# Kernel optimization log

Measured on AMD Instinct MI355X. Metric: run time of the kernel, lower is better.

The kernel has to match this reference:

```python
import jax, jax.numpy as jnp
import numpy as np

N_SEND = 100000   # sender nodes
N_RECV = 100000   # receiver nodes
E = 600000        # edges
D = 128           # node feature channels (128x0e)
A = 8             # attr channels (8x0e)
S = 64            # edge scalar dim = fc_neurons[0]
H = 128           # fc hidden = fc_neurons[1]; tp.weight_numel = 128
NUM_NEIGHBORS = 32.0
SILU_NORM = 1.679177  # e3nn normalize2mom constant for silu: (E[silu(N(0,1))^2])^-0.5


def fctp(x, y, W):
    """e3nn FullyConnectedTensorProduct for all-scalar (0e) irreps:
    single 'uvw' path, path weight 1/sqrt(mul_u*mul_v)."""
    return jnp.einsum('nu,nv,uvw->nw', x, y, W) / np.sqrt(x.shape[1] * y.shape[1]).astype(np.float32)


def setup_inputs() -> dict:
    key = jax.random.key(0)
    ks = jax.random.split(key, 14)
    return {
        'sender_input': jax.random.normal(ks[0], (N_SEND, D), jnp.float32),
        'sender_attr': jax.random.normal(ks[1], (N_SEND, A), jnp.float32),
        'receiver_input': jax.random.normal(ks[2], (N_RECV, D), jnp.float32),
        'receiver_attr': jax.random.normal(ks[3], (N_RECV, A), jnp.float32),
        'edge_src': jax.random.randint(ks[4], (E,), 0, N_SEND, jnp.int32),
        'edge_dst': jax.random.randint(ks[5], (E,), 0, N_RECV, jnp.int32),
        'edge_attr': jax.random.normal(ks[6], (E, 1), jnp.float32),
        'edge_scalars': jax.random.normal(ks[7], (E, S), jnp.float32),
        # e3nn TP weights are initialized N(0,1)
        'W_sc': jax.random.normal(ks[8], (D, A, D), jnp.float32),
        'W_lin1': jax.random.normal(ks[9], (D, A, D), jnp.float32),
        'W_fc1': jax.random.normal(ks[10], (S, H), jnp.float32),
        'W_fc2': jax.random.normal(ks[11], (H, D), jnp.float32),
        'W_lin2': jax.random.normal(ks[12], (D, A, D), jnp.float32),
        'W_lin3': jax.random.normal(ks[13], (D, A, 1), jnp.float32),
    }


def reference(sender_input, sender_attr, receiver_input, receiver_attr,
              edge_src, edge_dst, edge_attr, edge_scalars,
              W_sc, W_lin1, W_fc1, W_fc2, W_lin2, W_lin3):
    # FullyConnectedNet([S, H, weight_numel], silu): act(x@W/sqrt(fan_in)), last layer linear
    h = SILU_NORM * jax.nn.silu(edge_scalars @ W_fc1 / np.sqrt(S).astype(np.float32))
    weight = h @ W_fc2 / np.sqrt(H).astype(np.float32)                     # [E, D] per-edge TP weights

    receiver_self_connection = fctp(receiver_input, receiver_attr, W_sc)   # [Nr, D]
    sender_features = fctp(sender_input, sender_attr, W_lin1)              # [Ns, D]

    # gather -> per-edge weighted ('uvu') tensor product with 1x0e edge_attr -> scatter-add
    edge_features = weight * sender_features[edge_src] * edge_attr         # [E, D]
    receiver_features = jax.ops.segment_sum(edge_features, edge_dst,
                                            num_segments=receiver_input.shape[0])
    receiver_features = receiver_features / np.sqrt(NUM_NEIGHBORS).astype(np.float32)

    receiver_conv_out = fctp(receiver_features, receiver_attr, W_lin2)     # [Nr, D]
    receiver_angle = 0.1 * fctp(receiver_features, receiver_attr, W_lin3)  # [Nr, 1]
    # sc.output_mask is all-ones for this irreps config, so sin gating applies to all channels
    return jnp.cos(receiver_angle) * receiver_self_connection + jnp.sin(receiver_angle) * receiver_conv_out
```

## Files before the change

### kernel.cpp

```cpp
#include <hip/hip_runtime.h>
#include <hip/hip_bf16.h>
#include <math.h>

#define NS 100000
#define NR 100000
#define NE 600000
#define SILU_NORM 1.679177f

typedef __attribute__((ext_vector_type(8))) short short8;
typedef __attribute__((ext_vector_type(4))) float f32x4;

static __device__ __forceinline__ short f2bf(float f) {
    return __builtin_bit_cast(short, __float2bfloat16(f));
}

#define GLDS16(g, l)                                                         \
    __builtin_amdgcn_global_load_lds(                                        \
        (const __attribute__((address_space(1))) unsigned int*)(const void*)(g), \
        (__attribute__((address_space(3))) unsigned int*)(void*)(l), 16, 0, 0)

__global__ void swz_kernel(const float* __restrict__ W,
                           __hip_bfloat16* __restrict__ out, int total)
{
    int idx = blockIdx.x * 256 + threadIdx.x;
    if (idx >= total) return;
    int s = idx >> 12, r = idx & 4095;
    int f = r >> 9;  r &= 511;
    int quad = r >> 7; r &= 127;
    int wl = r >> 3;
    int j = r & 7;
    int k = s * 32 + quad * 8 + j;
    int w = f * 16 + wl;
    out[idx] = __float2bfloat16(W[(size_t)k * 128 + w]);
}

__global__ __launch_bounds__(256) void hist_kernel(const int* __restrict__ edst,
                                                   int* __restrict__ cnt)
{
    int i = blockIdx.x * 256 + threadIdx.x;
    if (i < NE) atomicAdd(&cnt[edst[i]], 1);
}

#define SCAN_BLK 1024

__global__ __launch_bounds__(256) void scan1_kernel(const int* __restrict__ cnt,
                                                    int* __restrict__ bsum, int n)
{
    __shared__ int ts[256];
    int b = blockIdx.x, t = threadIdx.x;
    int base = b * SCAN_BLK + t * 4;
    int s = 0;
    #pragma unroll
    for (int k = 0; k < 4; ++k) { int i = base + k; if (i < n) s += cnt[i]; }
    ts[t] = s; __syncthreads();
    #pragma unroll
    for (int off = 128; off; off >>= 1) {
        if (t < off) ts[t] += ts[t + off];
        __syncthreads();
    }
    if (t == 0) bsum[b] = ts[0];
}

__global__ __launch_bounds__(128) void scan2_kernel(const int* __restrict__ bsum,
                                                    int* __restrict__ bofs, int nb)
{
    __shared__ int sh[128];
    int t = threadIdx.x;
    sh[t] = (t < nb) ? bsum[t] : 0;
    __syncthreads();
    for (int off = 1; off < 128; off <<= 1) {
        int v = (t >= off) ? sh[t - off] : 0;
        __syncthreads();
        sh[t] += v;
        __syncthreads();
    }
    if (t < nb) bofs[t] = (t == 0) ? 0 : sh[t - 1];
}

__global__ __launch_bounds__(256) void scan3_kernel(const int* __restrict__ cnt,
                                                    const int* __restrict__ bofs,
                                                    int* __restrict__ ofs, int n)
{
    __shared__ int ts[256];
    int b = blockIdx.x, t = threadIdx.x;
    int base = b * SCAN_BLK + t * 4;
    int v[4]; int s = 0;
    #pragma unroll
    for (int k = 0; k < 4; ++k) {
        int i = base + k;
        v[k] = (i < n) ? cnt[i] : 0;
        s += v[k];
    }
    ts[t] = s; __syncthreads();
    for (int off = 1; off < 256; off <<= 1) {
        int u = (t >= off) ? ts[t - off] : 0;
        __syncthreads();
        ts[t] += u;
        __syncthreads();
    }
    int run = bofs[b] + ts[t] - s;
    #pragma unroll
    for (int k = 0; k < 4; ++k) {
        int i = base + k;
        if (i < n) ofs[i] = run;
        run += v[k];
    }
}

__global__ __launch_bounds__(256) void scatter_kernel(const int* __restrict__ edst,
                                                      int* __restrict__ ofs,
                                                      int* __restrict__ perm)
{
    int i = blockIdx.x * 256 + threadIdx.x;
    if (i < NE) {
        int pos = atomicAdd(&ofs[edst[i]], 1);
        perm[pos] = i;
    }
}

__global__ __launch_bounds__(256) void fctp_mfma_kernel(
    const float* __restrict__ x, const float* __restrict__ y,
    const __hip_bfloat16* __restrict__ Wswz, float* __restrict__ out,
    float scale, int N)
{
    __shared__ __hip_bfloat16 Wb[2][8192];
    __shared__ float xs[2][128 * 8];

    const int tid = threadIdx.x;
    const int lane = tid & 63;
    const int wv = tid >> 6;
    const int quad = lane >> 4;
    const int wl = lane & 15;
    const int n0 = blockIdx.x * 128;

    float ya[2][8];
    #pragma unroll
    for (int mt = 0; mt < 2; ++mt) {
        int node = n0 + wv * 32 + mt * 16 + wl;
        if (node >= N) node = N - 1;
        const float4* yp = (const float4*)(y + (size_t)node * 8);
        float4 a = yp[0], b = yp[1];
        ya[mt][0] = a.x; ya[mt][1] = a.y; ya[mt][2] = a.z; ya[mt][3] = a.w;
        ya[mt][4] = b.x; ya[mt][5] = b.y; ya[mt][6] = b.z; ya[mt][7] = b.w;
    }

    f32x4 acc[2][8];
    #pragma unroll
    for (int mt = 0; mt < 2; ++mt)
        #pragma unroll
        for (int f = 0; f < 8; ++f)
            acc[mt][f] = (f32x4){0.f, 0.f, 0.f, 0.f};

    auto stage = [&](int b, int cc) {
        const char* src = (const char*)(Wswz + (size_t)cc * 8192);
        #pragma unroll
        for (int i = 0; i < 4; ++i) {
            int off = (i * 256 + tid) * 16;
            GLDS16(src + off, (char*)Wb[b] + off);
        }
        int nl = tid >> 1, c4 = (tid & 1) * 4;
        int node = n0 + nl;
        if (node >= N) node = N - 1;
        GLDS16(x + (size_t)node * 128 + cc * 8 + c4, (char*)xs[b] + tid * 16);
    };

    stage(0, 0);
    __syncthreads();

    for (int cc = 0; cc < 16; ++cc) {
        int cur = cc & 1;
        if (cc < 15) stage(cur ^ 1, cc + 1);

        #pragma unroll
        for (int ks = 0; ks < 2; ++ks) {
            short8 bfr[8];
            #pragma unroll
            for (int f = 0; f < 8; ++f)
                bfr[f] = *(const short8*)((const short*)Wb[cur] +
                                          (size_t)ks * 4096 + (f * 64 + lane) * 8);
            #pragma unroll
            for (int mt = 0; mt < 2; ++mt) {
                float xv = xs[cur][(wv * 32 + mt * 16 + wl) * 8 + ks * 4 + quad];
                short8 af;
                #pragma unroll
                for (int v = 0; v < 8; ++v) af[v] = f2bf(xv * ya[mt][v]);
                #pragma unroll
                for (int f = 0; f < 8; ++f)
                    acc[mt][f] = __builtin_amdgcn_mfma_f32_16x16x32_bf16(
                        af, bfr[f], acc[mt][f], 0, 0, 0);
            }
        }
        __syncthreads();
    }

    #pragma unroll
    for (int mt = 0; mt < 2; ++mt) {
        #pragma unroll
        for (int r = 0; r < 4; ++r) {
            int node = n0 + wv * 32 + mt * 16 + quad * 4 + r;
            if (node < N) {
                #pragma unroll
                for (int f = 0; f < 8; ++f)
                    out[(size_t)node * 128 + f * 16 + wl] = acc[mt][f][r] * scale;
            }
        }
    }
}

__global__ __launch_bounds__(256, 4) void edge_mfma_kernel(
    const int* __restrict__ esrc, const int* __restrict__ edst,
    const float* __restrict__ eattr, const float* __restrict__ escal,
    const int* __restrict__ perm,
    const __hip_bfloat16* __restrict__ W1swz,
    const __hip_bfloat16* __restrict__ W2swz,
    const float* __restrict__ sf, float* __restrict__ rfeat)
{
    __shared__ __hip_bfloat16 hA[16384];

    const int tid = threadIdx.x;
    const int lane = tid & 63;
    const int wv = tid >> 6;
    const int quad = lane >> 4;
    const int wl = lane & 15;
    const int e0 = blockIdx.x * 128;

    int epm[2];
    #pragma unroll
    for (int mt = 0; mt < 2; ++mt) {
        int j = e0 + (wv * 2 + mt) * 16 + wl;
        if (j >= NE) j = NE - 1;
        epm[mt] = perm[j];
    }

    short8 af1[2][2];
    #pragma unroll
    for (int ks = 0; ks < 2; ++ks)
        #pragma unroll
        for (int mt = 0; mt < 2; ++mt) {
            const float4* p = (const float4*)(escal + (size_t)epm[mt] * 64 +
                                              ks * 32 + quad * 8);
            float4 a = p[0], b = p[1];
            short8 v;
            v[0] = f2bf(a.x); v[1] = f2bf(a.y); v[2] = f2bf(a.z); v[3] = f2bf(a.w);
            v[4] = f2bf(b.x); v[5] = f2bf(b.y); v[6] = f2bf(b.z); v[7] = f2bf(b.w);
            af1[ks][mt] = v;
        }

    f32x4 acc1[2][8];
    #pragma unroll
    for (int mt = 0; mt < 2; ++mt)
        #pragma unroll
        for (int f = 0; f < 8; ++f) acc1[mt][f] = (f32x4){0.f, 0.f, 0.f, 0.f};

    #pragma unroll
    for (int ks = 0; ks < 2; ++ks)
        #pragma unroll
        for (int f = 0; f < 8; ++f) {
            short8 bfr = *(const short8*)((const short*)W1swz +
                                          (size_t)ks * 4096 + (f * 64 + lane) * 8);
            acc1[0][f] = __builtin_amdgcn_mfma_f32_16x16x32_bf16(
                af1[0][0], bfr, acc1[0][f], 0, 0, 0);
            acc1[1][f] = __builtin_amdgcn_mfma_f32_16x16x32_bf16(
                af1[0][1], bfr, acc1[1][f], 0, 0, 0);
        }

    #pragma unroll
    for (int mt = 0; mt < 2; ++mt)
        #pragma unroll
        for (int f = 0; f < 8; ++f) acc1[mt][f] = (f32x4){0.f, 0.f, 0.f, 0.f};
    #pragma unroll
    for (int ks = 0; ks < 2; ++ks)
        #pragma unroll
        for (int f = 0; f < 8; ++f) {
            short8 bfr = *(const short8*)((const short*)W1swz +
                                          (size_t)ks * 4096 + (f * 64 + lane) * 8);
            acc1[0][f] = __builtin_amdgcn_mfma_f32_16x16x32_bf16(
                af1[ks][0], bfr, acc1[0][f], 0, 0, 0);
            acc1[1][f] = __builtin_amdgcn_mfma_f32_16x16x32_bf16(
                af1[ks][1], bfr, acc1[1][f], 0, 0, 0);
        }

    #pragma unroll
    for (int mt = 0; mt < 2; ++mt) {
        int MT = wv * 2 + mt;
        #pragma unroll
        for (int f = 0; f < 8; ++f) {
            int s2 = f >> 1;
            int q2 = ((f & 1) * 2 + (wl >> 3)) & 3;
            int j2 = wl & 7;
            #pragma unroll
            for (int r = 0; r < 4; ++r) {
                float t = acc1[mt][f][r] * 0.125f;
                float h = SILU_NORM * t / (1.f + __expf(-t));
                int lpos = q2 * 16 + quad * 4 + r;
                ((short*)hA)[((size_t)(s2 * 8 + MT) * 64 + lpos) * 8 + j2] = f2bf(h);
            }
        }
    }
    __syncthreads();

    f32x4 acc2[2][8];
    #pragma unroll
    for (int mt = 0; mt < 2; ++mt)
        #pragma unroll
        for (int f = 0; f < 8; ++f) acc2[mt][f] = (f32x4){0.f, 0.f, 0.f, 0.f};

    #pragma unroll
    for (int ks = 0; ks < 4; ++ks) {
        short8 afA = *(const short8*)((const short*)hA +
                                      ((size_t)(ks * 8 + wv * 2 + 0) * 64 + lane) * 8);
        short8 afB = *(const short8*)((const short*)hA +
                                      ((size_t)(ks * 8 + wv * 2 + 1) * 64 + lane) * 8);
        #pragma unroll
        for (int f = 0; f < 8; ++f) {
            short8 bfr = *(const short8*)((const short*)W2swz +
                                          (size_t)ks * 4096 + (f * 64 + lane) * 8);
            acc2[0][f] = __builtin_amdgcn_mfma_f32_16x16x32_bf16(
                afA, bfr, acc2[0][f], 0, 0, 0);
            acc2[1][f] = __builtin_amdgcn_mfma_f32_16x16x32_bf16(
                afB, bfr, acc2[1][f], 0, 0, 0);
        }
    }

    const float s128 = 0.08838834764831845f;
    #pragma unroll
    for (int mt = 0; mt < 2; ++mt) {
        int jbase = e0 + (wv * 2 + mt) * 16 + quad * 4;
        if (jbase < NE) {
            int4 pj = *(const int4*)(perm + jbase);
            int dsts[4], srcs[4];
            float eas[4];
            #pragma unroll
            for (int r = 0; r < 4; ++r) {
                int e = (r == 0) ? pj.x : (r == 1) ? pj.y : (r == 2) ? pj.z : pj.w;
                dsts[r] = edst[e];
                srcs[r] = esrc[e];
                eas[r]  = eattr[e] * s128;
            }
            float run[8];
            int curdst = dsts[0];
            #pragma unroll
            for (int f = 0; f < 8; ++f)
                run[f] = acc2[mt][f][0] * eas[0] *
                         sf[(size_t)srcs[0] * 128 + f * 16 + wl];
            #pragma unroll
            for (int r = 1; r < 4; ++r) {
                float val[8];
                #pragma unroll
                for (int f = 0; f < 8; ++f)
                    val[f] = acc2[mt][f][r] * eas[r] *
                             sf[(size_t)srcs[r] * 128 + f * 16 + wl];
                if (dsts[r] == curdst) {
                    #pragma unroll
                    for (int f = 0; f < 8; ++f) run[f] += val[f];
                } else {
                    #pragma unroll
                    for (int f = 0; f < 8; ++f)
                        atomicAdd(&rfeat[(size_t)curdst * 128 + f * 16 + wl], run[f]);
                    curdst = dsts[r];
                    #pragma unroll
                    for (int f = 0; f < 8; ++f) run[f] = val[f];
                }
            }
            #pragma unroll
            for (int f = 0; f < 8; ++f)
                atomicAdd(&rfeat[(size_t)curdst * 128 + f * 16 + wl], run[f]);
        }
    }
}

__global__ __launch_bounds__(256) void conv_fuse_kernel(
    const float* __restrict__ x, const float* __restrict__ y,
    const __hip_bfloat16* __restrict__ Wswz, const float* __restrict__ W3,
    const float* __restrict__ rsc, float* __restrict__ out, int N)
{
    __shared__ __hip_bfloat16 Wb[2][8192];
    __shared__ float xs[2][128 * 8];

    const int tid = threadIdx.x;
    const int lane = tid & 63;
    const int wv = tid >> 6;
    const int quad = lane >> 4;
    const int wl = lane & 15;
    const int n0 = blockIdx.x * 128;

    float ya[2][8];
    #pragma unroll
    for (int mt = 0; mt < 2; ++mt) {
        int node = n0 + wv * 32 + mt * 16 + wl;
        if (node >= N) node = N - 1;
        const float4* yp = (const float4*)(y + (size_t)node * 8);
        float4 a = yp[0], b = yp[1];
        ya[mt][0] = a.x; ya[mt][1] = a.y; ya[mt][2] = a.z; ya[mt][3] = a.w;
        ya[mt][4] = b.x; ya[mt][5] = b.y; ya[mt][6] = b.z; ya[mt][7] = b.w;
    }

    f32x4 acc[2][8];
    #pragma unroll
    for (int mt = 0; mt < 2; ++mt)
        #pragma unroll
        for (int f = 0; f < 8; ++f)
            acc[mt][f] = (f32x4){0.f, 0.f, 0.f, 0.f};
    float aacc[2] = {0.f, 0.f};

    auto stage = [&](int b, int cc) {
        const char* src = (const char*)(Wswz + (size_t)cc * 8192);
        #pragma unroll
        for (int i = 0; i < 4; ++i) {
            int off = (i * 256 + tid) * 16;
            GLDS16(src + off, (char*)Wb[b] + off);
        }
        int nl = tid >> 1, c4 = (tid & 1) * 4;
        int node = n0 + nl;
        if (node >= N) node = N - 1;
        GLDS16(x + (size_t)node * 128 + cc * 8 + c4, (char*)xs[b] + tid * 16);
    };

    stage(0, 0);
    __syncthreads();

    for (int cc = 0; cc < 16; ++cc) {
        int cur = cc & 1;
        if (cc < 15) stage(cur ^ 1, cc + 1);

        #pragma unroll
        for (int ks = 0; ks < 2; ++ks) {
            short8 bfr[8];
            #pragma unroll
            for (int f = 0; f < 8; ++f)
                bfr[f] = *(const short8*)((const short*)Wb[cur] +
                                          (size_t)ks * 4096 + (f * 64 + lane) * 8);
            const float4* wp = (const float4*)(W3 + ((cc * 8 + ks * 4 + quad) * 8));
            float4 w3a = wp[0], w3b = wp[1];
            float w3v[8] = {w3a.x, w3a.y, w3a.z, w3a.w, w3b.x, w3b.y, w3b.z, w3b.w};
            #pragma unroll
            for (int mt = 0; mt < 2; ++mt) {
                float xv = xs[cur][(wv * 32 + mt * 16 + wl) * 8 + ks * 4 + quad];
                short8 af;
                #pragma unroll
                for (int v = 0; v < 8; ++v) {
                    float pr = xv * ya[mt][v];
                    af[v] = f2bf(pr);
                    aacc[mt] += pr * w3v[v];
                }
                #pragma unroll
                for (int f = 0; f < 8; ++f)
                    acc[mt][f] = __builtin_amdgcn_mfma_f32_16x16x32_bf16(
                        af, bfr[f], acc[mt][f], 0, 0, 0);
            }
        }
        __syncthreads();
    }

    float ared[2];
    #pragma unroll
    for (int mt = 0; mt < 2; ++mt) {
        float a = aacc[mt];
        a += __shfl_xor(a, 16);
        a += __shfl_xor(a, 32);
        ared[mt] = a * 5.524271728019903e-4f;
    }

    const float cs = 5.524271728019903e-3f;
    #pragma unroll
    for (int mt = 0; mt < 2; ++mt) {
        #pragma unroll
        for (int r = 0; r < 4; ++r) {
            int node = n0 + wv * 32 + mt * 16 + quad * 4 + r;
            float a = __shfl(ared[mt], quad * 4 + r);
            if (node < N) {
                float ca = __cosf(a), sa = __sinf(a);
                #pragma unroll
                for (int f = 0; f < 8; ++f) {
                    size_t o = (size_t)node * 128 + f * 16 + wl;
                    out[o] = ca * rsc[o] + sa * (acc[mt][f][r] * cs);
                }
            }
        }
    }
}

extern "C" void kernel_launch(void* const* d_in, const int* in_sizes, int n_in,
                              void* d_out, int out_size, void* d_ws, size_t ws_size,
                              hipStream_t stream)
{
    const float* sender_input   = (const float*)d_in[0];
    const float* sender_attr    = (const float*)d_in[1];
    const float* receiver_input = (const float*)d_in[2];
    const float* receiver_attr  = (const float*)d_in[3];
    const int*   edge_src  = (const int*)d_in[4];
    const int*   edge_dst  = (const int*)d_in[5];
    const float* edge_attr = (const float*)d_in[6];
    const float* edge_scal = (const float*)d_in[7];
    const float* W_sc   = (const float*)d_in[8];
    const float* W_lin1 = (const float*)d_in[9];
    const float* W_fc1  = (const float*)d_in[10];
    const float* W_fc2  = (const float*)d_in[11];
    const float* W_lin2 = (const float*)d_in[12];
    const float* W_lin3 = (const float*)d_in[13];

    char* ws = (char*)d_ws;
    float* sf    = (float*)(ws);
    float* rfeat = (float*)(ws + 51200000);
    __hip_bfloat16* Wl1s = (__hip_bfloat16*)(ws + 102400000);
    __hip_bfloat16* Wscs = (__hip_bfloat16*)(ws + 102662144);
    __hip_bfloat16* Wl2s = (__hip_bfloat16*)(ws + 102924288);
    __hip_bfloat16* W1s  = (__hip_bfloat16*)(ws + 103186432);
    __hip_bfloat16* W2s  = (__hip_bfloat16*)(ws + 103202816);
    float* rsc = sf;

    int* perm = (int*)d_out;
    int* cnt  = (int*)d_out + 600000;
    int* ofs  = (int*)d_out + 700000;
    int* bsum = (int*)d_out + 800000;
    int* bofs = (int*)d_out + 800128;

    swz_kernel<<<512, 256, 0, stream>>>(W_lin1, Wl1s, 131072);
    swz_kernel<<<512, 256, 0, stream>>>(W_sc,   Wscs, 131072);
    swz_kernel<<<512, 256, 0, stream>>>(W_lin2, Wl2s, 131072);
    swz_kernel<<<32,  256, 0, stream>>>(W_fc1,  W1s,  8192);
    swz_kernel<<<64,  256, 0, stream>>>(W_fc2,  W2s,  16384);

    hipMemsetAsync(rfeat, 0, (size_t)NR * 128 * 4, stream);
    hipMemsetAsync(cnt, 0, (size_t)NR * 4, stream);

    const int nbScan = (NR + SCAN_BLK - 1) / SCAN_BLK;
    hist_kernel<<<(NE + 255) / 256, 256, 0, stream>>>(edge_dst, cnt);
    scan1_kernel<<<nbScan, 256, 0, stream>>>(cnt, bsum, NR);
    scan2_kernel<<<1, 128, 0, stream>>>(bsum, bofs, nbScan);
    scan3_kernel<<<nbScan, 256, 0, stream>>>(cnt, bofs, ofs, NR);
    scatter_kernel<<<(NE + 255) / 256, 256, 0, stream>>>(edge_dst, ofs, perm);

    fctp_mfma_kernel<<<(NS + 127) / 128, 256, 0, stream>>>(
        sender_input, sender_attr, Wl1s, sf, 0.03125f, NS);
    edge_mfma_kernel<<<(NE + 127) / 128, 256, 0, stream>>>(
        edge_src, edge_dst, edge_attr, edge_scal, perm, W1s, W2s, sf, rfeat);
    fctp_mfma_kernel<<<(NR + 127) / 128, 256, 0, stream>>>(
        receiver_input, receiver_attr, Wscs, rsc, 0.03125f, NR);
    conv_fuse_kernel<<<(NR + 127) / 128, 256, 0, stream>>>(
        rfeat, receiver_attr, Wl2s, W_lin3, rsc, (float*)d_out, NR);
}
```

Baseline: 698.3 us.

## Keep edge MLP hidden in registers via transposed MFMA, pre-sort edge metadata

Computes the first FC layer transposed (weights as A operand) so the SiLU output lands directly in the register layout needed as the A fragment of the second MFMA, with W_fc2 re-swizzled to match. This removes the shared-memory staging buffer and the block barrier. The scatter kernel now also writes dst, src and edge_attr in sorted order, so the edge kernel reads them with contiguous vector loads instead of gathering through perm. The duplicated first-layer MFMA pass is removed, sender-feature gathers are issued up front, and launch bounds drop to 3 blocks per SM to give more registers.

```diff
diff --git a/kernel.cpp b/kernel.cpp
--- a/kernel.cpp
+++ b/kernel.cpp
@@ -34,6 +34,21 @@
     out[idx] = __float2bfloat16(W[(size_t)k * 128 + w]);
 }
 
+__global__ void swz2pi_kernel(const float* __restrict__ W,
+                              __hip_bfloat16* __restrict__ out, int total)
+{
+    int idx = blockIdx.x * 256 + threadIdx.x;
+    if (idx >= total) return;
+    int s = idx >> 12, r = idx & 4095;
+    int f = r >> 9;  r &= 511;
+    int quad = r >> 7; r &= 127;
+    int wl = r >> 3;
+    int j = r & 7;
+    int c = 32 * s + 16 * (j >> 2) + 4 * quad + (j & 3);
+    int w = f * 16 + wl;
+    out[idx] = __float2bfloat16(W[(size_t)c * 128 + w]);
+}
+
 __global__ __launch_bounds__(256) void hist_kernel(const int* __restrict__ edst,
                                                    int* __restrict__ cnt)
 {
@@ -107,14 +122,20 @@
     }
 }
 
-__global__ __launch_bounds__(256) void scatter_kernel(const int* __restrict__ edst,
-                                                      int* __restrict__ ofs,
-                                                      int* __restrict__ perm)
+__global__ __launch_bounds__(256) void scatter_kernel(
+    const int* __restrict__ edst, const int* __restrict__ esrc,
+    const float* __restrict__ eattr, int* __restrict__ ofs,
+    int* __restrict__ perm, int* __restrict__ edst_s,
+    int* __restrict__ esrc_s, float* __restrict__ eattr_s)
 {
     int i = blockIdx.x * 256 + threadIdx.x;
     if (i < NE) {
-        int pos = atomicAdd(&ofs[edst[i]], 1);
+        int d = edst[i];
+        int pos = atomicAdd(&ofs[d], 1);
         perm[pos] = i;
+        edst_s[pos] = d;
+        esrc_s[pos] = esrc[i];
+        eattr_s[pos] = eattr[i];
     }
 }
 
@@ -207,16 +228,14 @@
     }
 }
 
-__global__ __launch_bounds__(256, 4) void edge_mfma_kernel(
-    const int* __restrict__ esrc, const int* __restrict__ edst,
-    const float* __restrict__ eattr, const float* __restrict__ escal,
-    const int* __restrict__ perm,
+__global__ __launch_bounds__(256, 3) void edge_mfma_kernel(
+    const int* __restrict__ perm, const int* __restrict__ edst_s,
+    const int* __restrict__ esrc_s, const float* __restrict__ eattr_s,
+    const float* __restrict__ escal,
     const __hip_bfloat16* __restrict__ W1swz,
     const __hip_bfloat16* __restrict__ W2swz,
     const float* __restrict__ sf, float* __restrict__ rfeat)
 {
-    __shared__ __hip_bfloat16 hA[16384];
-
     const int tid = threadIdx.x;
     const int lane = tid & 63;
     const int wv = tid >> 6;
@@ -230,6 +249,20 @@
         int j = e0 + (wv * 2 + mt) * 16 + wl;
         if (j >= NE) j = NE - 1;
         epm[mt] = perm[j];
+    }
+
+    const float s128 = 0.08838834764831845f;
+    int4 dstv[2], srcv[2];
+    float4 eav[2];
+    bool valid[2];
+    #pragma unroll
+    for (int mt = 0; mt < 2; ++mt) {
+        int jb = e0 + (wv * 2 + mt) * 16 + quad * 4;
+        valid[mt] = (jb < NE);
+        int jc = valid[mt] ? jb : 0;
+        dstv[mt] = *(const int4*)(edst_s + jc);
+        srcv[mt] = *(const int4*)(esrc_s + jc);
+        eav[mt]  = *(const float4*)(eattr_s + jc);
     }
 
     short8 af1[2][2];
@@ -246,110 +279,72 @@
             af1[ks][mt] = v;
         }
 
-    f32x4 acc1[2][8];
-    #pragma unroll
-    for (int mt = 0; mt < 2; ++mt)
-        #pragma unroll
-        for (int f = 0; f < 8; ++f) acc1[mt][f] = (f32x4){0.f, 0.f, 0.f, 0.f};
-
-    #pragma unroll
-    for (int ks = 0; ks < 2; ++ks)
-        #pragma unroll
-        for (int f = 0; f < 8; ++f) {
-            short8 bfr = *(const short8*)((const short*)W1swz +
-                                          (size_t)ks * 4096 + (f * 64 + lane) * 8);
-            acc1[0][f] = __builtin_amdgcn_mfma_f32_16x16x32_bf16(
-                af1[0][0], bfr, acc1[0][f], 0, 0, 0);
-            acc1[1][f] = __builtin_amdgcn_mfma_f32_16x16x32_bf16(
-                af1[0][1], bfr, acc1[1][f], 0, 0, 0);
-        }
-
-    #pragma unroll
-    for (int mt = 0; mt < 2; ++mt)
-        #pragma unroll
-        for (int f = 0; f < 8; ++f) acc1[mt][f] = (f32x4){0.f, 0.f, 0.f, 0.f};
-    #pragma unroll
-    for (int ks = 0; ks < 2; ++ks)
-        #pragma unroll
-        for (int f = 0; f < 8; ++f) {
-            short8 bfr = *(const short8*)((const short*)W1swz +
-                                          (size_t)ks * 4096 + (f * 64 + lane) * 8);
-            acc1[0][f] = __builtin_amdgcn_mfma_f32_16x16x32_bf16(
-                af1[ks][0], bfr, acc1[0][f], 0, 0, 0);
-            acc1[1][f] = __builtin_amdgcn_mfma_f32_16x16x32_bf16(
-                af1[ks][1], bfr, acc1[1][f], 0, 0, 0);
-        }
-
-    #pragma unroll
-    for (int mt = 0; mt < 2; ++mt) {
-        int MT = wv * 2 + mt;
-        #pragma unroll
-        for (int f = 0; f < 8; ++f) {
-            int s2 = f >> 1;
-            int q2 = ((f & 1) * 2 + (wl >> 3)) & 3;
-            int j2 = wl & 7;
-            #pragma unroll
-            for (int r = 0; r < 4; ++r) {
-                float t = acc1[mt][f][r] * 0.125f;
-                float h = SILU_NORM * t / (1.f + __expf(-t));
-                int lpos = q2 * 16 + quad * 4 + r;
-                ((short*)hA)[((size_t)(s2 * 8 + MT) * 64 + lpos) * 8 + j2] = f2bf(h);
-            }
-        }
-    }
-    __syncthreads();
-
-    f32x4 acc2[2][8];
-    #pragma unroll
-    for (int mt = 0; mt < 2; ++mt)
-        #pragma unroll
-        for (int f = 0; f < 8; ++f) acc2[mt][f] = (f32x4){0.f, 0.f, 0.f, 0.f};
-
-    #pragma unroll
-    for (int ks = 0; ks < 4; ++ks) {
-        short8 afA = *(const short8*)((const short*)hA +
-                                      ((size_t)(ks * 8 + wv * 2 + 0) * 64 + lane) * 8);
-        short8 afB = *(const short8*)((const short*)hA +
-                                      ((size_t)(ks * 8 + wv * 2 + 1) * 64 + lane) * 8);
-        #pragma unroll
-        for (int f = 0; f < 8; ++f) {
-            short8 bfr = *(const short8*)((const short*)W2swz +
-                                          (size_t)ks * 4096 + (f * 64 + lane) * 8);
-            acc2[0][f] = __builtin_amdgcn_mfma_f32_16x16x32_bf16(
-                afA, bfr, acc2[0][f], 0, 0, 0);
-            acc2[1][f] = __builtin_amdgcn_mfma_f32_16x16x32_bf16(
-                afB, bfr, acc2[1][f], 0, 0, 0);
-        }
-    }
-
-    const float s128 = 0.08838834764831845f;
-    #pragma unroll
-    for (int mt = 0; mt < 2; ++mt) {
-        int jbase = e0 + (wv * 2 + mt) * 16 + quad * 4;
-        if (jbase < NE) {
-            int4 pj = *(const int4*)(perm + jbase);
-            int dsts[4], srcs[4];
-            float eas[4];
-            #pragma unroll
-            for (int r = 0; r < 4; ++r) {
-                int e = (r == 0) ? pj.x : (r == 1) ? pj.y : (r == 2) ? pj.z : pj.w;
-                dsts[r] = edst[e];
-                srcs[r] = esrc[e];
-                eas[r]  = eattr[e] * s128;
-            }
+    #pragma unroll
+    for (int mt = 0; mt < 2; ++mt) {
+        f32x4 acc1[8];
+        #pragma unroll
+        for (int f = 0; f < 8; ++f) acc1[f] = (f32x4){0.f, 0.f, 0.f, 0.f};
+        #pragma unroll
+        for (int ks = 0; ks < 2; ++ks)
+            #pragma unroll
+            for (int f = 0; f < 8; ++f) {
+                short8 wf = *(const short8*)((const short*)W1swz +
+                                             (size_t)ks * 4096 + (f * 64 + lane) * 8);
+                acc1[f] = __builtin_amdgcn_mfma_f32_16x16x32_bf16(
+                    wf, af1[ks][mt], acc1[f], 0, 0, 0);
+            }
+
+        short8 af2[4];
+        #pragma unroll
+        for (int ks = 0; ks < 4; ++ks) {
+            #pragma unroll
+            for (int half = 0; half < 2; ++half) {
+                int f = 2 * ks + half;
+                #pragma unroll
+                for (int r = 0; r < 4; ++r) {
+                    float t = acc1[f][r] * 0.125f;
+                    float h = SILU_NORM * t / (1.f + __expf(-t));
+                    af2[ks][half * 4 + r] = f2bf(h);
+                }
+            }
+        }
+
+        f32x4 acc2[8];
+        #pragma unroll
+        for (int f = 0; f < 8; ++f) acc2[f] = (f32x4){0.f, 0.f, 0.f, 0.f};
+        #pragma unroll
+        for (int ks = 0; ks < 4; ++ks)
+            #pragma unroll
+            for (int f = 0; f < 8; ++f) {
+                short8 wf = *(const short8*)((const short*)W2swz +
+                                             (size_t)ks * 4096 + (f * 64 + lane) * 8);
+                acc2[f] = __builtin_amdgcn_mfma_f32_16x16x32_bf16(
+                    af2[ks], wf, acc2[f], 0, 0, 0);
+            }
+
+        if (valid[mt]) {
+            int dsts[4] = {dstv[mt].x, dstv[mt].y, dstv[mt].z, dstv[mt].w};
+            int srcs[4] = {srcv[mt].x, srcv[mt].y, srcv[mt].z, srcv[mt].w};
+            float eas[4] = {eav[mt].x * s128, eav[mt].y * s128,
+                            eav[mt].z * s128, eav[mt].w * s128};
+            float g[4][8];
+            #pragma unroll
+            for (int r = 0; r < 4; ++r)
+                #pragma unroll
+                for (int f = 0; f < 8; ++f)
+                    g[r][f] = sf[(size_t)srcs[r] * 128 + f * 16 + wl];
+
             float run[8];
             int curdst = dsts[0];
             #pragma unroll
             for (int f = 0; f < 8; ++f)
-                run[f] = acc2[mt][f][0] * eas[0] *
-                         sf[(size_t)srcs[0] * 128 + f * 16 + wl];
+                run[f] = acc2[f][0] * eas[0] * g[0][f];
             #pragma unroll
             for (int r = 1; r < 4; ++r) {
                 float val[8];
                 #pragma unroll
                 for (int f = 0; f < 8; ++f)
-                    val[f] = acc2[mt][f][r] * eas[r] *
-                             sf[(size_t)srcs[r] * 128 + f * 16 + wl];
+                    val[f] = acc2[f][r] * eas[r] * g[r][f];
                 if (dsts[r] == curdst) {
                     #pragma unroll
                     for (int f = 0; f < 8; ++f) run[f] += val[f];
@@ -509,17 +504,20 @@
     __hip_bfloat16* W2s  = (__hip_bfloat16*)(ws + 103202816);
     float* rsc = sf;
 
-    int* perm = (int*)d_out;
-    int* cnt  = (int*)d_out + 600000;
-    int* ofs  = (int*)d_out + 700000;
-    int* bsum = (int*)d_out + 800000;
-    int* bofs = (int*)d_out + 800128;
+    int*   perm    = (int*)d_out;
+    int*   edst_s  = (int*)d_out + 600000;
+    int*   esrc_s  = (int*)d_out + 1200000;
+    float* eattr_s = (float*)d_out + 1800000;
+    int*   cnt     = (int*)d_out + 2400000;
+    int*   ofs     = (int*)d_out + 2500000;
+    int*   bsum    = (int*)d_out + 2600000;
+    int*   bofs    = (int*)d_out + 2600128;
 
     swz_kernel<<<512, 256, 0, stream>>>(W_lin1, Wl1s, 131072);
     swz_kernel<<<512, 256, 0, stream>>>(W_sc,   Wscs, 131072);
     swz_kernel<<<512, 256, 0, stream>>>(W_lin2, Wl2s, 131072);
     swz_kernel<<<32,  256, 0, stream>>>(W_fc1,  W1s,  8192);
-    swz_kernel<<<64,  256, 0, stream>>>(W_fc2,  W2s,  16384);
+    swz2pi_kernel<<<64, 256, 0, stream>>>(W_fc2, W2s,  16384);
 
     hipMemsetAsync(rfeat, 0, (size_t)NR * 128 * 4, stream);
     hipMemsetAsync(cnt, 0, (size_t)NR * 4, stream);
@@ -529,12 +527,13 @@
     scan1_kernel<<<nbScan, 256, 0, stream>>>(cnt, bsum, NR);
     scan2_kernel<<<1, 128, 0, stream>>>(bsum, bofs, nbScan);
     scan3_kernel<<<nbScan, 256, 0, stream>>>(cnt, bofs, ofs, NR);
-    scatter_kernel<<<(NE + 255) / 256, 256, 0, stream>>>(edge_dst, ofs, perm);
+    scatter_kernel<<<(NE + 255) / 256, 256, 0, stream>>>(
+        edge_dst, edge_src, edge_attr, ofs, perm, edst_s, esrc_s, eattr_s);
 
     fctp_mfma_kernel<<<(NS + 127) / 128, 256, 0, stream>>>(
         sender_input, sender_attr, Wl1s, sf, 0.03125f, NS);
     edge_mfma_kernel<<<(NE + 127) / 128, 256, 0, stream>>>(
-        edge_src, edge_dst, edge_attr, edge_scal, perm, W1s, W2s, sf, rfeat);
+        perm, edst_s, esrc_s, eattr_s, edge_scal, W1s, W2s, sf, rfeat);
     fctp_mfma_kernel<<<(NR + 127) / 128, 256, 0, stream>>>(
         receiver_input, receiver_attr, Wscs, rsc, 0.03125f, NR);
     conv_fuse_kernel<<<(NR + 127) / 128, 256, 0, stream>>>(
```

After: 715.8 us. 2.5% more time.
